# Kernel optimization log

Hardware: AMD Instinct MI355X
Metric: run time of the kernel (lower is better)

## Reference

```python
import jax, jax.numpy as jnp
import numpy as np

B, T, D, H, W = 4, 2048, 256, 512, 32
EPS = 1e-5


def _xavier(key, fan_in, fan_out):
    # torch xavier_uniform on weight [out, in]; stored here as [in, out]
    limit = float(np.sqrt(6.0 / (fan_in + fan_out)))
    return jax.random.uniform(key, (fan_in, fan_out), jnp.float32, -limit, limit)


def _bias(key, fan_in, fan_out):
    # torch Linear default bias init: U(-1/sqrt(fan_in), 1/sqrt(fan_in))
    limit = float(1.0 / np.sqrt(fan_in))
    return jax.random.uniform(key, (fan_out,), jnp.float32, -limit, limit)


def setup_inputs() -> dict:
    key = jax.random.key(0)
    ks = jax.random.split(key, 16)
    inp = {
        "feature": jax.random.normal(ks[0], (B, T, D), jnp.float32),
        "gamma": jnp.ones((D,), jnp.float32),
        "beta": jnp.zeros((D,), jnp.float32),
        "w1": _xavier(ks[1], D, H), "b1": _bias(ks[2], D, H),
        "w2": _xavier(ks[3], H, H), "b2": _bias(ks[4], H, H),
        "w3": _xavier(ks[5], D, H), "b3": _bias(ks[6], H, H),
        "w4": _xavier(ks[7], H, H), "b4": _bias(ks[8], H, H),
        "w5": _xavier(ks[9], D, H), "b5": _bias(ks[10], H, H),
        "w6": _xavier(ks[11], H, H), "b6": _bias(ks[12], H, H),
        "window": W,
    }
    return inp


def reference(feature, gamma, beta, w1, b1, w2, b2, w3, b3, w4, b4, w5, b5, w6, b6, window):
    Bsz, Tlen, Din = feature.shape
    nb = Tlen // window
    x = feature.reshape(Bsz, nb, window, Din)  # [B, nb, W, D] window blocks

    # LayerNorm over last dim
    mu = jnp.mean(x, axis=-1, keepdims=True)
    var = jnp.mean((x - mu) ** 2, axis=-1, keepdims=True)
    n = (x - mu) * jax.lax.rsqrt(var + EPS) * gamma + beta

    Q = jnp.tanh(n @ w1 + b1) @ w2 + b2  # [B, nb, W, H]
    K = jnp.tanh(n @ w3 + b3) @ w4 + b4
    V = jax.nn.relu(n @ w5 + b5) @ w6 + b6

    Hdim = w2.shape[1]
    sqrt_feat = jnp.sqrt(jnp.float32(Hdim))
    sqrt_time = jnp.sqrt(jnp.float32(window))

    # time-axis attention: [B, nb, W, W]
    beta_time = jnp.einsum('bnwh,bnvh->bnwv', Q, K) / sqrt_feat
    # feature-axis attention: [B, nb, H, H]
    beta_feat = jnp.einsum('bnwh,bnwg->bnhg', Q, K) / sqrt_time

    A_time = jax.nn.softmax(beta_time, axis=-1)
    A_feat = jax.nn.softmax(beta_feat, axis=-2)

    feat = jnp.einsum('bnwh,bnhg->bnwg', V, A_feat)   # V @ A_feat
    out = jnp.einsum('bnwv,bnvg->bnwg', A_time, feat)  # A_time @ (V @ A_feat)
    return out.reshape(Bsz, Tlen, Hdim)
```

## Files before the change

### kernel.cpp

```cpp
#include <hip/hip_runtime.h>
#include <hip/hip_bf16.h>

typedef unsigned short u16;
typedef __attribute__((ext_vector_type(8))) unsigned short ushort8;
typedef __attribute__((ext_vector_type(8))) short short8;
typedef __attribute__((ext_vector_type(4))) float f32x4;
typedef __attribute__((ext_vector_type(4))) unsigned uint4_t;

#define DEV __device__ __forceinline__

DEV float b2f(u16 u){ return __uint_as_float(((unsigned)u) << 16); }
DEV u16 f2b(float f){
  unsigned x = __float_as_uint(f);
  return (u16)((x + 0x7fffu + ((x >> 16) & 1u)) >> 16);
}
DEV unsigned cvtpk(float lo, float hi){
  unsigned r;
  asm("v_cvt_pk_bf16_f32 %0, %1, %2" : "=v"(r) : "v"(lo), "v"(hi));
  return r;
}
DEV void pl32swap(unsigned& a, unsigned& b){
  asm("v_permlane32_swap_b32 %0, %1" : "+v"(a), "+v"(b));
}
DEV void pl16swap(unsigned& a, unsigned& b){
  asm("v_permlane16_swap_b32 %0, %1" : "+v"(a), "+v"(b));
}
DEV float fexp2(float x){
  float r;
  asm("v_exp_f32 %0, %1" : "=v"(r) : "v"(x));
  return r;
}
DEV float frcp(float x){
  float r;
  asm("v_rcp_f32 %0, %1" : "=v"(r) : "v"(x));
  return r;
}
DEV short8 ld8(const u16* p){ return __builtin_bit_cast(short8, *(const ushort8*)p); }
DEV f32x4 mfma(short8 a, short8 b, f32x4 c){
  return __builtin_amdgcn_mfma_f32_16x16x32_bf16(a, b, c, 0, 0, 0);
}
DEV float fast_tanh(float x){
  float e = fexp2(x * 2.8853900817779268f);
  return 1.f - 2.f * frcp(e + 1.f);
}
DEV unsigned pk2(float lo, float hi){
  return (unsigned)f2b(lo) | ((unsigned)f2b(hi) << 16);
}

__global__ __launch_bounds__(256) void prep_k(
    const float* __restrict__ w1, const float* __restrict__ w2,
    const float* __restrict__ w3, const float* __restrict__ w4,
    const float* __restrict__ w5, const float* __restrict__ w6,
    u16* __restrict__ ws,
    const float* __restrict__ xg, const float* __restrict__ gg,
    const float* __restrict__ bgm, u16* __restrict__ ng)
{
  __shared__ u16 tile[64][72];
  const int bid = blockIdx.x;
  if (bid < 384) {
    const int z = bid / 64, rem = bid % 64, by = rem / 8, bx = rem % 8;
    const float* w; u16* wt; int K;
    switch (z) {
      case 0:  w = w1; wt = ws;          K = 256; break;
      case 1:  w = w2; wt = ws + 131072; K = 512; break;
      case 2:  w = w3; wt = ws + 393216; K = 256; break;
      case 3:  w = w4; wt = ws + 524288; K = 512; break;
      case 4:  w = w5; wt = ws + 786432; K = 256; break;
      default: w = w6; wt = ws + 917504; K = 512; break;
    }
    int k0 = by * 64;
    if (k0 >= K) return;
    int n0 = bx * 64;
    int t = threadIdx.x;
    int r = t >> 2, c0 = (t & 3) * 16;
    const float* src = w + (size_t)(k0 + r) * 512 + n0 + c0;
    #pragma unroll
    for (int jj = 0; jj < 4; ++jj) {
      float4 v = *(const float4*)(src + jj * 4);
      unsigned* tp = (unsigned*)&tile[r][c0 + jj*4];
      tp[0] = cvtpk(v.x, v.y);
      tp[1] = cvtpk(v.z, v.w);
    }
    __syncthreads();
    ushort8 o0, o1;
    #pragma unroll
    for (int j = 0; j < 8; ++j) { o0[j] = tile[c0 + j][r]; o1[j] = tile[c0 + 8 + j][r]; }
    u16* dst = wt + (size_t)(n0 + r) * K + k0 + c0;
    *(ushort8*)dst       = o0;
    *(ushort8*)(dst + 8) = o1;
  } else {
    const int lb = bid - 384;
    int row = lb * 8 + (threadIdx.x >> 5);
    int l32 = threadIdx.x & 31;
    const float* xr = xg + (size_t)row*256 + l32*8;
    float xf[8];
    #pragma unroll
    for (int j = 0; j < 8; j += 4) {
      float4 v = *(const float4*)(xr + j);
      xf[j] = v.x; xf[j+1] = v.y; xf[j+2] = v.z; xf[j+3] = v.w;
    }
    float s = 0.f, ss = 0.f;
    #pragma unroll
    for (int j = 0; j < 8; ++j){ s += xf[j]; ss += xf[j]*xf[j]; }
    #pragma unroll
    for (int m = 1; m < 32; m <<= 1){ s += __shfl_xor(s, m); ss += __shfl_xor(ss, m); }
    float mean = s * (1.f/256.f);
    float var  = ss * (1.f/256.f) - mean*mean;
    float rs   = rsqrtf(var + 1e-5f);
    float r8[8];
    #pragma unroll
    for (int j = 0; j < 8; j += 4) {
      float4 gv = *(const float4*)(gg  + l32*8 + j);
      float4 bv = *(const float4*)(bgm + l32*8 + j);
      r8[j]   = (xf[j]   - mean)*rs*gv.x + bv.x;
      r8[j+1] = (xf[j+1] - mean)*rs*gv.y + bv.y;
      r8[j+2] = (xf[j+2] - mean)*rs*gv.z + bv.z;
      r8[j+3] = (xf[j+3] - mean)*rs*gv.w + bv.w;
    }
    uint4_t o;
    o[0] = cvtpk(r8[0], r8[1]); o[1] = cvtpk(r8[2], r8[3]);
    o[2] = cvtpk(r8[4], r8[5]); o[3] = cvtpk(r8[6], r8[7]);
    *(uint4_t*)(ng + (size_t)row*256 + l32*8) = o;
  }
}

template<int NS, int ACT>
__global__ __launch_bounds__(512, 4) void gemm_tile(
    const u16* __restrict__ Abase, size_t a_zstride,
    const u16* __restrict__ wst, int w_off0,
    const float* __restrict__ bz0, const float* __restrict__ bz1, const float* __restrict__ bz2,
    u16* __restrict__ Cbase)
{
  constexpr int KA = NS * 32;
  __shared__ __align__(16) u16 sm[20480];
  u16* smA = sm;
  u16* smB = sm + 10240;
  const int z = blockIdx.z;
  const u16* A = Abase + (size_t)z * a_zstride;
  const u16* W = wst + w_off0 + z * 393216;
  const float* bias = (z == 0) ? bz0 : ((z == 1) ? bz1 : bz2);
  u16* C = Cbase + (size_t)z * 4194304;
  const int M0 = blockIdx.x * 128, N0 = blockIdx.y * 128;
  const int tid = threadIdx.x;
  const int wv = tid >> 6, ln = tid & 63, q = ln >> 4, r16 = ln & 15;
  const int m0w = (wv >> 2) * 64, n0w = (wv & 3) * 32;
  const f32x4 Z = {0.f, 0.f, 0.f, 0.f};

  const int srow = tid >> 2, scq = (tid & 3) * 8;
  const u16* gA = A + (size_t)(M0 + srow) * KA + scq;
  const u16* gB = W + (size_t)(N0 + srow) * KA + scq;
  u16* dA = smA + srow * 40 + scq;
  u16* dB = smB + srow * 40 + scq;

  ushort8 rA[2], rB[2];
  rA[0] = *(const ushort8*)gA;
  rB[0] = *(const ushort8*)gB;
  *(ushort8*)dA = rA[0];
  *(ushort8*)dB = rB[0];
  if (NS > 1) { rA[1] = *(const ushort8*)(gA + 32); rB[1] = *(const ushort8*)(gB + 32); }
  __syncthreads();

  f32x4 acc[4][2];
  #pragma unroll
  for (int mf = 0; mf < 4; ++mf){ acc[mf][0] = Z; acc[mf][1] = Z; }

  #pragma unroll
  for (int kk = 0; kk < NS; ++kk) {
    const int cur = kk & 1;
    const u16* bufA = smA + cur * 5120;
    const u16* bufB = smB + cur * 5120;
    short8 aF[4], bF[2];
    #pragma unroll
    for (int mf = 0; mf < 4; ++mf) aF[mf] = ld8(bufA + (m0w + mf*16 + r16)*40 + q*8);
    #pragma unroll
    for (int nf = 0; nf < 2; ++nf) bF[nf] = ld8(bufB + (n0w + nf*16 + r16)*40 + q*8);
    #pragma unroll
    for (int mf = 0; mf < 4; ++mf)
      #pragma unroll
      for (int nf = 0; nf < 2; ++nf)
        acc[mf][nf] = mfma(aF[mf], bF[nf], acc[mf][nf]);
    if (kk + 1 < NS) {
      *(ushort8*)(dA + (cur ^ 1) * 5120) = rA[(kk + 1) & 1];
      *(ushort8*)(dB + (cur ^ 1) * 5120) = rB[(kk + 1) & 1];
    }
    if (kk + 2 < NS) {
      rA[kk & 1] = *(const ushort8*)(gA + (kk + 2) * 32);
      rB[kk & 1] = *(const ushort8*)(gB + (kk + 2) * 32);
    }
    __syncthreads();
  }

  u16* ct = sm;
  #pragma unroll
  for (int nf = 0; nf < 2; ++nf) {
    int colL = n0w + nf*16 + r16;
    float bs = bias[N0 + colL];
    #pragma unroll
    for (int mf = 0; mf < 4; ++mf)
      #pragma unroll
      for (int i = 0; i < 4; ++i) {
        int row = m0w + mf*16 + q*4 + i;
        float v = acc[mf][nf][i] + bs;
        if (ACT == 1) v = fmaxf(v, 0.f);
        else if (ACT == 3) v = (z == 2) ? fmaxf(v, 0.f) : fast_tanh(v);
        ct[row*132 + colL] = f2b(v);
      }
  }
  __syncthreads();
  #pragma unroll
  for (int j = 0; j < 4; ++j) {
    int row = (tid >> 4) + j*32;
    int cb2 = (tid & 15) * 8;
    ushort8 vv = *(const ushort8*)(ct + row*132 + cb2);
    *(ushort8*)(C + (size_t)(M0 + row)*512 + N0 + cb2) = vv;
  }
}

#define AV   0
#define AQT  16640
#define AKT  37120
#define ABT  57600
#define AAT  59712
#define ASM_ELS 60992

__global__ __launch_bounds__(1024) void attn_k(
    const u16* __restrict__ QKVg, float* __restrict__ outg)
{
  __shared__ __align__(16) u16 sm[ASM_ELS];
  const int tid = threadIdx.x;
  const int bid = blockIdx.x;
  const int wv = tid >> 6, ln = tid & 63, q = ln >> 4, r16 = ln & 15;
  const f32x4 Z = {0.f, 0.f, 0.f, 0.f};
  const float RS512 = 0.04419417382415922f;
  const float C32L2 = 0.25500526676986233f;
  const u16* Qg = QKVg + (size_t)bid * 16384;
  const u16* Kg = QKVg + 4194304 + (size_t)bid * 16384;
  const u16* Vg = QKVg + 8388608 + (size_t)bid * 16384;

  float* btf = (float*)(sm + ABT);
  if (wv < 4) {
    int mt = wv >> 1, nt = wv & 1;
    f32x4 acc = Z;
    const u16* qb = Qg + (mt*16 + r16)*512;
    const u16* kb = Kg + (nt*16 + r16)*512;
    #pragma unroll
    for (int kk = 0; kk < 16; ++kk)
      acc = mfma(ld8(qb + kk*32 + q*8), ld8(kb + kk*32 + q*8), acc);
    #pragma unroll
    for (int i = 0; i < 4; ++i)
      btf[(mt*16 + q*4 + i)*33 + nt*16 + r16] = acc[i] * RS512;
  } else if (wv < 12) {
    int t1 = tid - 256;
    int rp = t1 & 15;
    int cb = (t1 >> 4) * 16;
    const u16* s0 = Qg + (2*rp)*512 + cb;
    const u16* s1 = s0 + 512;
    ushort8 a0 = *(const ushort8*)s0, a1 = *(const ushort8*)(s0 + 8);
    ushort8 c0v = *(const ushort8*)s1, c1v = *(const ushort8*)(s1 + 8);
    unsigned* qt32 = (unsigned*)(sm + AQT);
    #pragma unroll
    for (int j = 0; j < 8; ++j) {
      qt32[(cb + j)*20 + rp]     = (unsigned)a0[j] | ((unsigned)c0v[j] << 16);
      qt32[(cb + 8 + j)*20 + rp] = (unsigned)a1[j] | ((unsigned)c1v[j] << 16);
    }
  } else {
    int t2 = tid - 768;
    int vrow = t2 >> 3, seg = (t2 & 7) * 64;
    const u16* src = Vg + vrow*512 + seg;
    #pragma unroll
    for (int jj = 0; jj < 8; ++jj)
      *(ushort8*)(sm + AV + vrow*520 + seg + jj*8) = *(const ushort8*)(src + jj*8);
  }
  __syncthreads();

  if (tid < 512) {
    int row = tid >> 4, v2 = tid & 15;
    float v0 = btf[row*33 + v2], v1 = btf[row*33 + v2 + 16];
    float m = fmaxf(v0, v1);
    #pragma unroll
    for (int msk = 1; msk < 16; msk <<= 1) m = fmaxf(m, __shfl_xor(m, msk));
    float e0 = __expf(v0 - m), e1 = __expf(v1 - m);
    float sum = e0 + e1;
    #pragma unroll
    for (int msk = 1; msk < 16; msk <<= 1) sum += __shfl_xor(sum, msk);
    float inv = 1.f / sum;
    sm[AAT + row*40 + v2]      = f2b(e0 * inv);
    sm[AAT + row*40 + v2 + 16] = f2b(e1 * inv);
  } else {
    int t1 = tid - 512;
    int rp = t1 & 15;
    int cb = (t1 >> 4) * 16;
    const u16* s0 = Kg + (2*rp)*512 + cb;
    const u16* s1 = s0 + 512;
    ushort8 a0 = *(const ushort8*)s0, a1 = *(const ushort8*)(s0 + 8);
    ushort8 c0v = *(const ushort8*)s1, c1v = *(const ushort8*)(s1 + 8);
    unsigned* kt32 = (unsigned*)(sm + AKT);
    #pragma unroll
    for (int j = 0; j < 8; ++j) {
      kt32[(cb + j)*20 + rp]     = (unsigned)a0[j] | ((unsigned)c0v[j] << 16);
      kt32[(cb + 8 + j)*20 + rp] = (unsigned)a1[j] | ((unsigned)c1v[j] << 16);
    }
  }
  __syncthreads();

  {
    const int g0 = wv * 32;
    f32x4 facc[2][2];
    facc[0][0]=Z; facc[0][1]=Z; facc[1][0]=Z; facc[1][1]=Z;
    float csum[2] = {0.f, 0.f};
    short8 bK[2];
    #pragma unroll
    for (int gt = 0; gt < 2; ++gt)
      bK[gt] = ld8(sm + AKT + (size_t)(g0 + gt*16 + r16)*40 + q*8);

    #pragma unroll 2
    for (int ht = 0; ht < 16; ++ht) {
      f32x4 sv[2][2];
      #pragma unroll
      for (int smi = 0; smi < 2; ++smi) {
        short8 aQ = ld8(sm + AQT + (ht*32 + smi*16 + r16)*40 + q*8);
        #pragma unroll
        for (int gt = 0; gt < 2; ++gt)
          sv[smi][gt] = mfma(aQ, bK[gt], Z);
      }
      unsigned D[2][4];
      #pragma unroll
      for (int gt = 0; gt < 2; ++gt) {
        float e[2][4];
        #pragma unroll
        for (int smi = 0; smi < 2; ++smi)
          #pragma unroll
          for (int i = 0; i < 4; ++i) {
            float ev = fexp2(sv[smi][gt][i] * C32L2);
            e[smi][i] = ev;
            csum[gt] += ev;
          }
        #pragma unroll
        for (int k = 0; k < 2; ++k) {
          unsigned w0 = cvtpk(e[0][2*k], e[0][2*k+1]);
          unsigned w1 = cvtpk(e[1][2*k], e[1][2*k+1]);
          pl32swap(w0, w1);
          pl16swap(w0, w1);
          D[gt][k]     = w0;
          D[gt][k + 2] = w1;
        }
      }
      #pragma unroll
      for (int mt = 0; mt < 2; ++mt) {
        short8 aV = ld8(sm + AV + (mt*16 + r16)*520 + ht*32 + q*8);
        #pragma unroll
        for (int gt = 0; gt < 2; ++gt) {
          uint4_t dv = {D[gt][0], D[gt][1], D[gt][2], D[gt][3]};
          short8 bE = __builtin_bit_cast(short8, dv);
          facc[mt][gt] = mfma(aV, bE, facc[mt][gt]);
        }
      }
    }
    float inv[2];
    #pragma unroll
    for (int gt = 0; gt < 2; ++gt) {
      float cs = csum[gt];
      cs += __shfl_xor(cs, 16);
      cs += __shfl_xor(cs, 32);
      inv[gt] = 1.f / cs;
    }
    unsigned F[2][4];
    #pragma unroll
    for (int gt = 0; gt < 2; ++gt) {
      float e0n[4], e1n[4];
      #pragma unroll
      for (int i = 0; i < 4; ++i) {
        e0n[i] = facc[0][gt][i] * inv[gt];
        e1n[i] = facc[1][gt][i] * inv[gt];
      }
      #pragma unroll
      for (int k = 0; k < 2; ++k) {
        unsigned w0 = cvtpk(e0n[2*k], e0n[2*k+1]);
        unsigned w1 = cvtpk(e1n[2*k], e1n[2*k+1]);
        pl32swap(w0, w1);
        pl16swap(w0, w1);
        F[gt][k]     = w0;
        F[gt][k + 2] = w1;
      }
    }
    short8 aA0 = ld8(sm + AAT + r16*40 + q*8);
    short8 aA1 = ld8(sm + AAT + (16 + r16)*40 + q*8);
    #pragma unroll
    for (int gt = 0; gt < 2; ++gt) {
      uint4_t fv = {F[gt][0], F[gt][1], F[gt][2], F[gt][3]};
      short8 bF = __builtin_bit_cast(short8, fv);
      f32x4 o0 = mfma(aA0, bF, Z);
      f32x4 o1 = mfma(aA1, bF, Z);
      #pragma unroll
      for (int i = 0; i < 4; ++i) {
        int g = g0 + gt*16 + r16;
        outg[(size_t)(bid*32 + q*4 + i)*512 + g]      = o0[i];
        outg[(size_t)(bid*32 + 16 + q*4 + i)*512 + g] = o1[i];
      }
    }
  }
}


#define OFF_V   0
#define OFF_N   16640
#define OFF_T   25088
#define OFF_Q   41728
#define OFF_K   58368
#define OFF_BT  75008
#define OFF_QT  16640
#define OFF_KT  37120
#define OFF_AT  78080
#define OFF_FT  37120
#define SMEM_ELS 79360

template<int ACT>
DEV void mlp_branch(const u16* __restrict__ nl, u16* __restrict__ tl, u16* __restrict__ ol,
                    const u16* __restrict__ wA, const float* __restrict__ bA,
                    const u16* __restrict__ wB, const float* __restrict__ bB,
                    int wv, int q, int r16)
{
  const f32x4 Z = {0.f, 0.f, 0.f, 0.f};
  const int c0 = wv*32 + r16;
  float biasA0 = bA[c0], biasA1 = bA[c0 + 16];
  float biasB0 = bB[c0], biasB1 = bB[c0 + 16];
  {
    const u16* cp0 = wA + (size_t)c0*256 + q*8;
    const u16* cp1 = cp0 + 16*256;
    const u16* a0p = nl + r16 * 264 + q*8;
    const u16* a1p = nl + (16 + r16) * 264 + q*8;
    f32x4 acc[2][2];
    acc[0][0]=Z; acc[0][1]=Z; acc[1][0]=Z; acc[1][1]=Z;
    #pragma unroll
    for (int kk = 0; kk < 8; ++kk) {
      short8 a0 = ld8(a0p + kk*32);
      short8 a1 = ld8(a1p + kk*32);
      short8 b0 = ld8(cp0 + kk*32);
      short8 b1 = ld8(cp1 + kk*32);
      acc[0][0] = mfma(a0, b0, acc[0][0]);
      acc[1][0] = mfma(a1, b0, acc[1][0]);
      acc[0][1] = mfma(a0, b1, acc[0][1]);
      acc[1][1] = mfma(a1, b1, acc[1][1]);
    }
    #pragma unroll
    for (int gt = 0; gt < 2; ++gt) {
      float bias = gt ? biasA1 : biasA0;
      #pragma unroll
      for (int mt = 0; mt < 2; ++mt)
        #pragma unroll
        for (int i = 0; i < 4; ++i) {
          float v = acc[mt][gt][i] + bias;
          v = (ACT == 0) ? fast_tanh(v) : fmaxf(v, 0.f);
          tl[(mt*16 + q*4 + i)*520 + c0 + gt*16] = f2b(v);
        }
    }
  }
  __syncthreads();
  {
    const u16* cp0 = wB + (size_t)c0*512 + q*8;
    const u16* cp1 = cp0 + 16*512;
    const u16* a0p = tl + r16 * 520 + q*8;
    const u16* a1p = tl + (16 + r16) * 520 + q*8;
    f32x4 acc[2][2];
    acc[0][0]=Z; acc[0][1]=Z; acc[1][0]=Z; acc[1][1]=Z;
    #pragma unroll
    for (int kk = 0; kk < 16; ++kk) {
      short8 a0 = ld8(a0p + kk*32);
      short8 a1 = ld8(a1p + kk*32);
      short8 b0 = ld8(cp0 + kk*32);
      short8 b1 = ld8(cp1 + kk*32);
      acc[0][0] = mfma(a0, b0, acc[0][0]);
      acc[1][0] = mfma(a1, b0, acc[1][0]);
      acc[0][1] = mfma(a0, b1, acc[0][1]);
      acc[1][1] = mfma(a1, b1, acc[1][1]);
    }
    #pragma unroll
    for (int gt = 0; gt < 2; ++gt) {
      float bias = gt ? biasB1 : biasB0;
      #pragma unroll
      for (int mt = 0; mt < 2; ++mt)
        #pragma unroll
        for (int i = 0; i < 4; ++i)
          ol[(mt*16 + q*4 + i)*520 + c0 + gt*16] = f2b(acc[mt][gt][i] + bias);
    }
  }
}

__global__ __launch_bounds__(1024) void fused_main(
    const float* __restrict__ xg, const float* __restrict__ gg, const float* __restrict__ bgm,
    const float* __restrict__ b1, const float* __restrict__ b2, const float* __restrict__ b3,
    const float* __restrict__ b4, const float* __restrict__ b5, const float* __restrict__ b6,
    const u16* __restrict__ wst, float* __restrict__ outg)
{
  __shared__ __align__(16) u16 sm[SMEM_ELS];
  const int tid = threadIdx.x;
  const int bid = blockIdx.x;
  const int wv = tid >> 6, ln = tid & 63, q = ln >> 4, r16 = ln & 15;
  const f32x4 Z = {0.f, 0.f, 0.f, 0.f};
  const float RS512 = 0.04419417382415922f;
  const float C32L2 = 0.25500526676986233f;

  {
    int row = tid >> 5, l32 = tid & 31;
    const float* xr = xg + (size_t)(bid*32 + row)*256 + l32*8;
    float xf[8];
    #pragma unroll
    for (int j = 0; j < 8; j += 4) {
      float4 v = *(const float4*)(xr + j);
      xf[j] = v.x; xf[j+1] = v.y; xf[j+2] = v.z; xf[j+3] = v.w;
    }
    float s = 0.f, ss = 0.f;
    #pragma unroll
    for (int j = 0; j < 8; ++j){ s += xf[j]; ss += xf[j]*xf[j]; }
    #pragma unroll
    for (int m = 1; m < 32; m <<= 1){ s += __shfl_xor(s, m); ss += __shfl_xor(ss, m); }
    float mean = s * (1.f/256.f);
    float var  = ss * (1.f/256.f) - mean*mean;
    float rs   = rsqrtf(var + 1e-5f);
    float gf[8], bf[8];
    #pragma unroll
    for (int j = 0; j < 8; j += 4) {
      float4 gv = *(const float4*)(gg  + l32*8 + j);
      float4 bv = *(const float4*)(bgm + l32*8 + j);
      gf[j] = gv.x; gf[j+1] = gv.y; gf[j+2] = gv.z; gf[j+3] = gv.w;
      bf[j] = bv.x; bf[j+1] = bv.y; bf[j+2] = bv.z; bf[j+3] = bv.w;
    }
    ushort8 o0;
    #pragma unroll
    for (int j = 0; j < 8; ++j)
      o0[j] = f2b((xf[j] - mean)*rs*gf[j] + bf[j]);
    *(ushort8*)(sm + OFF_N + row*264 + l32*8) = o0;
  }
  __syncthreads();

  mlp_branch<0>(sm+OFF_N, sm+OFF_T, sm+OFF_Q, wst,          b1, wst + 131072, b2, wv, q, r16);
  __syncthreads();
  mlp_branch<0>(sm+OFF_N, sm+OFF_T, sm+OFF_K, wst + 393216, b3, wst + 524288, b4, wv, q, r16);
  __syncthreads();
  mlp_branch<1>(sm+OFF_N, sm+OFF_T, sm+OFF_V, wst + 786432, b5, wst + 917504, b6, wv, q, r16);
  __syncthreads();

  float* btf = (float*)(sm + OFF_BT);
  if (wv < 4) {
    int mt = wv >> 1, nt = wv & 1;
    f32x4 acc = Z;
    const u16* qb = sm + OFF_Q + (mt*16 + r16)*520;
    const u16* kb = sm + OFF_K + (nt*16 + r16)*520;
    for (int kk = 0; kk < 16; ++kk)
      acc = mfma(ld8(qb + kk*32 + q*8), ld8(kb + kk*32 + q*8), acc);
    #pragma unroll
    for (int i = 0; i < 4; ++i)
      btf[(mt*16 + q*4 + i)*33 + nt*16 + r16] = acc[i] * RS512;
  } else if (wv < 12) {
    int t1 = tid - 256;
    int row = t1 & 31, cb = (t1 >> 5) * 32;
    const u16* src = sm + OFF_Q + row*520 + cb;
    ushort8 v[4];
    #pragma unroll
    for (int jj = 0; jj < 4; ++jj) v[jj] = *(const ushort8*)(src + jj*8);
    #pragma unroll
    for (int jj = 0; jj < 4; ++jj)
      #pragma unroll
      for (int j = 0; j < 8; ++j)
        sm[OFF_QT + (cb + jj*8 + j)*40 + row] = v[jj][j];
  }
  __syncthreads();

  if (tid < 512) {
    int row = tid >> 4, v2 = tid & 15;
    float v0 = btf[row*33 + v2], v1 = btf[row*33 + v2 + 16];
    float m = fmaxf(v0, v1);
    #pragma unroll
    for (int msk = 1; msk < 16; msk <<= 1) m = fmaxf(m, __shfl_xor(m, msk));
    float e0 = __expf(v0 - m), e1 = __expf(v1 - m);
    float sum = e0 + e1;
    #pragma unroll
    for (int msk = 1; msk < 16; msk <<= 1) sum += __shfl_xor(sum, msk);
    float inv = 1.f / sum;
    sm[OFF_AT + row*40 + v2]      = f2b(e0 * inv);
    sm[OFF_AT + row*40 + v2 + 16] = f2b(e1 * inv);
  } else {
    int t2 = tid - 512;
    int row = t2 & 31, cb = (t2 >> 5) * 32;
    const u16* src = sm + OFF_K + row*520 + cb;
    ushort8 v[4];
    #pragma unroll
    for (int jj = 0; jj < 4; ++jj) v[jj] = *(const ushort8*)(src + jj*8);
    #pragma unroll
    for (int jj = 0; jj < 4; ++jj)
      #pragma unroll
      for (int j = 0; j < 8; ++j)
        sm[OFF_KT + (cb + jj*8 + j)*40 + row] = v[jj][j];
  }
  __syncthreads();

  {
    const int g0 = wv * 32;
    const bool hi32 = (ln >= 32);
    const bool qodd = (q & 1);
    f32x4 facc[2][2];
    facc[0][0]=Z; facc[0][1]=Z; facc[1][0]=Z; facc[1][1]=Z;
    float csum[2] = {0.f, 0.f};
    short8 bK[2];
    #pragma unroll
    for (int gt = 0; gt < 2; ++gt)
      bK[gt] = ld8(sm + OFF_KT + (size_t)(g0 + gt*16 + r16)*40 + q*8);

    #pragma unroll 2
    for (int ht = 0; ht < 16; ++ht) {
      f32x4 sv[2][2];
      #pragma unroll
      for (int smi = 0; smi < 2; ++smi) {
        short8 aQ = ld8(sm + OFF_QT + (ht*32 + smi*16 + r16)*40 + q*8);
        #pragma unroll
        for (int gt = 0; gt < 2; ++gt)
          sv[smi][gt] = mfma(aQ, bK[gt], Z);
      }
      unsigned D[2][4];
      #pragma unroll
      for (int gt = 0; gt < 2; ++gt) {
        float e[2][4];
        #pragma unroll
        for (int smi = 0; smi < 2; ++smi)
          #pragma unroll
          for (int i = 0; i < 4; ++i) {
            float ev = fexp2(sv[smi][gt][i] * C32L2);
            e[smi][i] = ev;
            csum[gt] += ev;
          }
        #pragma unroll
        for (int k = 0; k < 2; ++k) {
          unsigned w0 = pk2(e[0][2*k], e[0][2*k+1]);
          unsigned w1 = pk2(e[1][2*k], e[1][2*k+1]);
          unsigned Pw0 = (unsigned)__shfl_xor((int)w0, 32);
          unsigned Pw1 = (unsigned)__shfl_xor((int)w1, 32);
          unsigned x = hi32 ? Pw1 : w0;
          unsigned y = hi32 ? w1 : Pw0;
          unsigned xs = (unsigned)__shfl_xor((int)x, 16);
          unsigned ys = (unsigned)__shfl_xor((int)y, 16);
          D[gt][k]     = qodd ? ys : x;
          D[gt][k + 2] = qodd ? y  : xs;
        }
      }
      #pragma unroll
      for (int mt = 0; mt < 2; ++mt) {
        short8 aV = ld8(sm + OFF_V + (mt*16 + r16)*520 + ht*32 + q*8);
        #pragma unroll
        for (int gt = 0; gt < 2; ++gt) {
          uint4_t dv = {D[gt][0], D[gt][1], D[gt][2], D[gt][3]};
          short8 bE = __builtin_bit_cast(short8, dv);
          facc[mt][gt] = mfma(aV, bE, facc[mt][gt]);
        }
      }
    }
    float inv[2];
    #pragma unroll
    for (int gt = 0; gt < 2; ++gt) {
      float cs = csum[gt];
      cs += __shfl_xor(cs, 16);
      cs += __shfl_xor(cs, 32);
      inv[gt] = 1.f / cs;
    }
    #pragma unroll
    for (int mt = 0; mt < 2; ++mt)
      #pragma unroll
      for (int gt = 0; gt < 2; ++gt)
        #pragma unroll
        for (int i = 0; i < 4; ++i) {
          int w = mt*16 + q*4 + i;
          int g = g0 + gt*16 + r16;
          sm[OFF_FT + g*40 + w] = f2b(facc[mt][gt][i] * inv[gt]);
        }
  }

  {
    const int g0 = wv * 32;
    short8 aA0 = ld8(sm + OFF_AT + r16*40 + q*8);
    short8 aA1 = ld8(sm + OFF_AT + (16 + r16)*40 + q*8);
    #pragma unroll
    for (int gt = 0; gt < 2; ++gt) {
      short8 bF = ld8(sm + OFF_FT + (size_t)(g0 + gt*16 + r16)*40 + q*8);
      f32x4 o0 = mfma(aA0, bF, Z);
      f32x4 o1 = mfma(aA1, bF, Z);
      #pragma unroll
      for (int i = 0; i < 4; ++i) {
        int g = g0 + gt*16 + r16;
        outg[(size_t)(bid*32 + q*4 + i)*512 + g]      = o0[i];
        outg[(size_t)(bid*32 + 16 + q*4 + i)*512 + g] = o1[i];
      }
    }
  }
}


extern "C" void kernel_launch(void* const* d_in, const int* in_sizes, int n_in,
                              void* d_out, int out_size, void* d_ws, size_t ws_size,
                              hipStream_t stream)
{
  const float* x  = (const float*)d_in[0];
  const float* gm = (const float*)d_in[1];
  const float* bt = (const float*)d_in[2];
  const float* w1 = (const float*)d_in[3];
  const float* b1 = (const float*)d_in[4];
  const float* w2 = (const float*)d_in[5];
  const float* b2 = (const float*)d_in[6];
  const float* w3 = (const float*)d_in[7];
  const float* b3 = (const float*)d_in[8];
  const float* w4 = (const float*)d_in[9];
  const float* b4 = (const float*)d_in[10];
  const float* w5 = (const float*)d_in[11];
  const float* b5 = (const float*)d_in[12];
  const float* w6 = (const float*)d_in[13];
  const float* b6 = (const float*)d_in[14];
  u16* ws  = (u16*)d_ws;
  float* out = (float*)d_out;

  const size_t WT_OFF  = 0;
  const size_t N_OFF   = 1179648;
  const size_t T_OFF   = 3276800;
  const size_t QKV_OFF = 15859712;
  const size_t NEED_BYTES = 28442624ULL * 2ULL;

  if (ws_size >= NEED_BYTES) {
    prep_k<<<1408, 256, 0, stream>>>(w1, w2, w3, w4, w5, w6, ws + WT_OFF,
                                     x, gm, bt, ws + N_OFF);
    gemm_tile<8, 3><<<dim3(64, 4, 3), 512, 0, stream>>>(
        ws + N_OFF, 0, ws + WT_OFF, 0, b1, b3, b5, ws + T_OFF);
    gemm_tile<16, 2><<<dim3(64, 4, 3), 512, 0, stream>>>(
        ws + T_OFF, 4194304, ws + WT_OFF, 131072, b2, b4, b6, ws + QKV_OFF);
    attn_k<<<256, 1024, 0, stream>>>(ws + QKV_OFF, out);
  } else {
    prep_k<<<384, 256, 0, stream>>>(w1, w2, w3, w4, w5, w6, ws + WT_OFF,
                                    x, gm, bt, ws + WT_OFF );
    fused_main<<<256, 1024, 0, stream>>>(x, gm, bt, b1, b2, b3, b4, b5, b6, ws + WT_OFF, out);
  }
}
```

Before: 71.41 us.

## Use 4-wave GEMM blocks with 64x64 warp tiles; prefetch Q fragments in attention

The GEMM tile kernel now uses 256 threads (4 waves) per 128x128 tile instead of 512. Each wave computes a 64x64 sub-tile with 16 accumulators, which raises MFMA-per-LDS-load reuse at the cost of more registers and lower occupancy. Each thread now loads and stores 16 elements per stage. In the attention kernel, the Q fragment LDS loads are software-prefetched one iteration ahead, and the small time-softmax uses exp2 and a fast reciprocal.

Result: no change. 72.40 us (+1.4%).

```diff
diff --git a/kernel.cpp b/kernel.cpp
--- a/kernel.cpp
+++ b/kernel.cpp
@@ -125,7 +125,7 @@
 }
 
 template<int NS, int ACT>
-__global__ __launch_bounds__(512, 4) void gemm_tile(
+__global__ __launch_bounds__(256, 3) void gemm_tile(
     const u16* __restrict__ Abase, size_t a_zstride,
     const u16* __restrict__ wst, int w_off0,
     const float* __restrict__ bz0, const float* __restrict__ bz1, const float* __restrict__ bz2,
@@ -143,56 +143,68 @@
   const int M0 = blockIdx.x * 128, N0 = blockIdx.y * 128;
   const int tid = threadIdx.x;
   const int wv = tid >> 6, ln = tid & 63, q = ln >> 4, r16 = ln & 15;
-  const int m0w = (wv >> 2) * 64, n0w = (wv & 3) * 32;
+  const int m0w = (wv >> 1) * 64, n0w = (wv & 1) * 64;
   const f32x4 Z = {0.f, 0.f, 0.f, 0.f};
 
-  const int srow = tid >> 2, scq = (tid & 3) * 8;
+  const int srow = tid >> 1, scq = (tid & 1) * 16;
   const u16* gA = A + (size_t)(M0 + srow) * KA + scq;
   const u16* gB = W + (size_t)(N0 + srow) * KA + scq;
   u16* dA = smA + srow * 40 + scq;
   u16* dB = smB + srow * 40 + scq;
 
-  ushort8 rA[2], rB[2];
-  rA[0] = *(const ushort8*)gA;
-  rB[0] = *(const ushort8*)gB;
-  *(ushort8*)dA = rA[0];
-  *(ushort8*)dB = rB[0];
-  if (NS > 1) { rA[1] = *(const ushort8*)(gA + 32); rB[1] = *(const ushort8*)(gB + 32); }
-  __syncthreads();
-
-  f32x4 acc[4][2];
+  ushort8 rA[2][2], rB[2][2];
+  rA[0][0] = *(const ushort8*)gA;       rA[0][1] = *(const ushort8*)(gA + 8);
+  rB[0][0] = *(const ushort8*)gB;       rB[0][1] = *(const ushort8*)(gB + 8);
+  *(ushort8*)dA       = rA[0][0];
+  *(ushort8*)(dA + 8) = rA[0][1];
+  *(ushort8*)dB       = rB[0][0];
+  *(ushort8*)(dB + 8) = rB[0][1];
+  if (NS > 1) {
+    rA[1][0] = *(const ushort8*)(gA + 32); rA[1][1] = *(const ushort8*)(gA + 40);
+    rB[1][0] = *(const ushort8*)(gB + 32); rB[1][1] = *(const ushort8*)(gB + 40);
+  }
+  __syncthreads();
+
+  f32x4 acc[4][4];
   #pragma unroll
-  for (int mf = 0; mf < 4; ++mf){ acc[mf][0] = Z; acc[mf][1] = Z; }
+  for (int mf = 0; mf < 4; ++mf)
+    #pragma unroll
+    for (int nf = 0; nf < 4; ++nf) acc[mf][nf] = Z;
 
   #pragma unroll
   for (int kk = 0; kk < NS; ++kk) {
     const int cur = kk & 1;
     const u16* bufA = smA + cur * 5120;
     const u16* bufB = smB + cur * 5120;
-    short8 aF[4], bF[2];
+    short8 aF[4], bF[4];
     #pragma unroll
     for (int mf = 0; mf < 4; ++mf) aF[mf] = ld8(bufA + (m0w + mf*16 + r16)*40 + q*8);
     #pragma unroll
-    for (int nf = 0; nf < 2; ++nf) bF[nf] = ld8(bufB + (n0w + nf*16 + r16)*40 + q*8);
+    for (int nf = 0; nf < 4; ++nf) bF[nf] = ld8(bufB + (n0w + nf*16 + r16)*40 + q*8);
     #pragma unroll
     for (int mf = 0; mf < 4; ++mf)
       #pragma unroll
-      for (int nf = 0; nf < 2; ++nf)
+      for (int nf = 0; nf < 4; ++nf)
         acc[mf][nf] = mfma(aF[mf], bF[nf], acc[mf][nf]);
     if (kk + 1 < NS) {
-      *(ushort8*)(dA + (cur ^ 1) * 5120) = rA[(kk + 1) & 1];
-      *(ushort8*)(dB + (cur ^ 1) * 5120) = rB[(kk + 1) & 1];
+      const int nxt = (kk + 1) & 1;
+      *(ushort8*)(dA + (cur ^ 1) * 5120)     = rA[nxt][0];
+      *(ushort8*)(dA + (cur ^ 1) * 5120 + 8) = rA[nxt][1];
+      *(ushort8*)(dB + (cur ^ 1) * 5120)     = rB[nxt][0];
+      *(ushort8*)(dB + (cur ^ 1) * 5120 + 8) = rB[nxt][1];
     }
     if (kk + 2 < NS) {
-      rA[kk & 1] = *(const ushort8*)(gA + (kk + 2) * 32);
-      rB[kk & 1] = *(const ushort8*)(gB + (kk + 2) * 32);
+      rA[kk & 1][0] = *(const ushort8*)(gA + (kk + 2) * 32);
+      rA[kk & 1][1] = *(const ushort8*)(gA + (kk + 2) * 32 + 8);
+      rB[kk & 1][0] = *(const ushort8*)(gB + (kk + 2) * 32);
+      rB[kk & 1][1] = *(const ushort8*)(gB + (kk + 2) * 32 + 8);
     }
     __syncthreads();
   }
 
   u16* ct = sm;
   #pragma unroll
-  for (int nf = 0; nf < 2; ++nf) {
+  for (int nf = 0; nf < 4; ++nf) {
     int colL = n0w + nf*16 + r16;
     float bs = bias[N0 + colL];
     #pragma unroll
@@ -208,8 +220,8 @@
   }
   __syncthreads();
   #pragma unroll
-  for (int j = 0; j < 4; ++j) {
-    int row = (tid >> 4) + j*32;
+  for (int j = 0; j < 8; ++j) {
+    int row = (tid >> 4) + j*16;
     int cb2 = (tid & 15) * 8;
     ushort8 vv = *(const ushort8*)(ct + row*132 + cb2);
     *(ushort8*)(C + (size_t)(M0 + row)*512 + N0 + cb2) = vv;
@@ -233,6 +245,7 @@
   const f32x4 Z = {0.f, 0.f, 0.f, 0.f};
   const float RS512 = 0.04419417382415922f;
   const float C32L2 = 0.25500526676986233f;
+  const float LOG2E = 1.4426950408889634f;
   const u16* Qg = QKVg + (size_t)bid * 16384;
   const u16* Kg = QKVg + 4194304 + (size_t)bid * 16384;
   const u16* Vg = QKVg + 8388608 + (size_t)bid * 16384;
@@ -279,11 +292,11 @@
     float m = fmaxf(v0, v1);
     #pragma unroll
     for (int msk = 1; msk < 16; msk <<= 1) m = fmaxf(m, __shfl_xor(m, msk));
-    float e0 = __expf(v0 - m), e1 = __expf(v1 - m);
+    float e0 = fexp2((v0 - m) * LOG2E), e1 = fexp2((v1 - m) * LOG2E);
     float sum = e0 + e1;
     #pragma unroll
     for (int msk = 1; msk < 16; msk <<= 1) sum += __shfl_xor(sum, msk);
-    float inv = 1.f / sum;
+    float inv = frcp(sum);
     sm[AAT + row*40 + v2]      = f2b(e0 * inv);
     sm[AAT + row*40 + v2 + 16] = f2b(e1 * inv);
   } else {
@@ -313,15 +326,21 @@
     for (int gt = 0; gt < 2; ++gt)
       bK[gt] = ld8(sm + AKT + (size_t)(g0 + gt*16 + r16)*40 + q*8);
 
+    short8 aQn0 = ld8(sm + AQT + (r16)*40 + q*8);
+    short8 aQn1 = ld8(sm + AQT + (16 + r16)*40 + q*8);
+
     #pragma unroll 2
     for (int ht = 0; ht < 16; ++ht) {
+      short8 aQ0 = aQn0, aQ1 = aQn1;
+      if (ht < 15) {
+        aQn0 = ld8(sm + AQT + ((ht+1)*32 + r16)*40 + q*8);
+        aQn1 = ld8(sm + AQT + ((ht+1)*32 + 16 + r16)*40 + q*8);
+      }
       f32x4 sv[2][2];
       #pragma unroll
-      for (int smi = 0; smi < 2; ++smi) {
-        short8 aQ = ld8(sm + AQT + (ht*32 + smi*16 + r16)*40 + q*8);
-        #pragma unroll
-        for (int gt = 0; gt < 2; ++gt)
-          sv[smi][gt] = mfma(aQ, bK[gt], Z);
+      for (int gt = 0; gt < 2; ++gt) {
+        sv[0][gt] = mfma(aQ0, bK[gt], Z);
+        sv[1][gt] = mfma(aQ1, bK[gt], Z);
       }
       unsigned D[2][4];
       #pragma unroll
@@ -724,9 +743,9 @@
   if (ws_size >= NEED_BYTES) {
     prep_k<<<1408, 256, 0, stream>>>(w1, w2, w3, w4, w5, w6, ws + WT_OFF,
                                      x, gm, bt, ws + N_OFF);
-    gemm_tile<8, 3><<<dim3(64, 4, 3), 512, 0, stream>>>(
+    gemm_tile<8, 3><<<dim3(64, 4, 3), 256, 0, stream>>>(
         ws + N_OFF, 0, ws + WT_OFF, 0, b1, b3, b5, ws + T_OFF);
-    gemm_tile<16, 2><<<dim3(64, 4, 3), 512, 0, stream>>>(
+    gemm_tile<16, 2><<<dim3(64, 4, 3), 256, 0, stream>>>(
         ws + T_OFF, 4194304, ws + WT_OFF, 131072, b2, b4, b6, ws + QKV_OFF);
     attn_k<<<256, 1024, 0, stream>>>(ws + QKV_OFF, out);
   } else {
```
